# Optimization experiments

Measured on AMD Instinct MI355X. Metric: run time of the kernel, lower is better.

Reference implementation:

```python
import jax, jax.numpy as jnp
import numpy as np

B, N, D_IN, D_OUT = 8, 2048, 256, 128
ROW_ZERO = 85 - 10  # hardcoded in original: a[:, 0:85-10] = 0 (zeros rows, dim 1)
NEG_BIG = -9.0e15
EPS = 1e-12  # F.normalize eps


def setup_inputs() -> dict:
    key = jax.random.key(0)
    k1, k2, k3, k4 = jax.random.split(key, 4)
    h = jax.random.normal(k1, (B, N, D_IN), dtype=jnp.float32)
    adj = jax.random.randint(k2, (B, N, N), 0, 2, dtype=jnp.int32)
    adj_eye = jax.random.randint(k3, (B, N, N), 0, 2, dtype=jnp.int32)
    # xavier_uniform with gain=1.414 for W [in, out]
    limit = 1.414 * np.sqrt(6.0 / (D_IN + D_OUT))
    W = jax.random.uniform(k4, (D_IN, D_OUT), minval=-limit, maxval=limit, dtype=jnp.float32)
    return {"h": h, "adj": adj, "adj_eye": adj_eye, "W": W}


def reference(h, adj, adj_eye, W):
    # Wh: [B, N, D_OUT]
    Wh = jnp.matmul(h, W)
    # L2-normalize along feature dim (F.normalize semantics: x / max(||x||, eps))
    norm = jnp.maximum(jnp.linalg.norm(Wh, axis=-1, keepdims=True), EPS)
    Whn = Wh / norm
    # dense cosine-similarity scores: [B, N, N]
    score = jnp.einsum("bnd,bmd->bnm", Whn, Whn)
    # double-sort top-k emulation (faithful to original, incl. row-wise zeroing bug)
    a_sorted = jnp.sort(score, axis=-1)
    idx1 = jnp.argsort(score, axis=-1)
    a_sorted = a_sorted.at[:, 0:ROW_ZERO, :].set(0.0)
    idx2 = jnp.argsort(idx1, axis=-1)  # inverse permutation
    attscore = jnp.take_along_axis(a_sorted, idx2, axis=-1)
    # adjacency mask + softmax over neighbors
    e = jnp.where(adj_eye > 0, attscore, NEG_BIG)
    attention = jax.nn.softmax(e, axis=-1)
    # (dropout is identity in eval mode)
    h_prime = jnp.matmul(attention, Wh)
    return jax.nn.elu(h_prime)
```

## Files before the change

kernel.cpp:

```cpp
#include <hip/hip_runtime.h>
#include <stdint.h>

#define NN   2048
#define DD   128
#define DIN  256
#define ROWZ 75

typedef float f32x4 __attribute__((ext_vector_type(4)));
typedef short bf16x8 __attribute__((ext_vector_type(8)));
typedef unsigned int u32x4 __attribute__((ext_vector_type(4)));
typedef unsigned int u32x2 __attribute__((ext_vector_type(2)));

__device__ __forceinline__ unsigned short f2bf(float x){
  union { float f; unsigned int u; } v; v.f = x;
  unsigned int u = v.u;
  u += 0x7fffu + ((u >> 16) & 1u);
  return (unsigned short)(u >> 16);
}
__device__ __forceinline__ float bf2f(unsigned short b){
  union { float f; unsigned int u; } v; v.u = ((unsigned int)b) << 16;
  return v.f;
}

__launch_bounds__(256, 2)
__global__ void wh_kernel(const float* __restrict__ h, const float* __restrict__ W,
                          unsigned short* __restrict__ whn, unsigned short* __restrict__ whT)
{
  __shared__ float hs[32][36];
  __shared__ float Ws[32][128];
  __shared__ float ssp[32][33];
  __shared__ float sinv[32];

  const int t  = threadIdx.x;
  const int r0 = blockIdx.x * 32;
  const int r4 = (t >> 5) * 4;
  const int d4 = (t & 31) * 4;

  float acc[4][4];
#pragma unroll
  for (int i = 0; i < 4; ++i)
#pragma unroll
    for (int j = 0; j < 4; ++j) acc[i][j] = 0.f;

  const int lrow = t >> 3;
  const int lkb  = (t & 7) * 4;

  for (int kt = 0; kt < 8; ++kt){
    __syncthreads();
    {
      const float* src = h + (size_t)(r0 + lrow) * DIN + kt * 32 + lkb;
      f32x4 a = *(const f32x4*)src;
#pragma unroll
      for (int e = 0; e < 4; ++e) hs[lkb + e][lrow] = a[e];
    }
    {
      const int k = t >> 3;
      const int d = (t & 7) * 16;
      const float* src = W + (size_t)(kt * 32 + k) * DD + d;
      float* dst = &Ws[k][d];
#pragma unroll
      for (int e = 0; e < 4; ++e) ((f32x4*)dst)[e] = ((const f32x4*)src)[e];
    }
    __syncthreads();
#pragma unroll
    for (int k = 0; k < 32; ++k){
      f32x4 w4 = *(const f32x4*)&Ws[k][d4];
      f32x4 ha = *(const f32x4*)&hs[k][r4];
#pragma unroll
      for (int i = 0; i < 4; ++i)
#pragma unroll
        for (int j = 0; j < 4; ++j)
          acc[i][j] += ha[i] * w4[j];
    }
  }

#pragma unroll
  for (int i = 0; i < 4; ++i){
    float s = acc[i][0]*acc[i][0] + acc[i][1]*acc[i][1]
            + acc[i][2]*acc[i][2] + acc[i][3]*acc[i][3];
    ssp[r4 + i][t & 31] = s;
  }
  __syncthreads();
  if (t < 32){
    float ss = 0.f;
#pragma unroll
    for (int c = 0; c < 32; ++c) ss += ssp[t][c];
    sinv[t] = 1.0f / fmaxf(sqrtf(ss), 1e-12f);
  }
  __syncthreads();

  const int bb = r0 >> 11;
  const int n0 = (r0 & 2047) + r4;

#pragma unroll
  for (int i = 0; i < 4; ++i){
    const float inv = sinv[r4 + i];
    unsigned int lo = (unsigned int)f2bf(acc[i][0]*inv) | ((unsigned int)f2bf(acc[i][1]*inv) << 16);
    unsigned int hi = (unsigned int)f2bf(acc[i][2]*inv) | ((unsigned int)f2bf(acc[i][3]*inv) << 16);
    u32x2 pk = { lo, hi };
    *(u32x2*)(whn + (size_t)(r0 + r4 + i) * DD + d4) = pk;
  }
#pragma unroll
  for (int j = 0; j < 4; ++j){
    u32x2 pk;
#pragma unroll
    for (int e = 0; e < 2; ++e)
      pk[e] = (unsigned int)f2bf(acc[2*e][j]) | ((unsigned int)f2bf(acc[2*e + 1][j]) << 16);
    *(u32x2*)(whT + ((size_t)(bb * DD + d4 + j)) * NN + n0) = pk;
  }
}

__launch_bounds__(256, 2)
__global__ void attn_kernel(const unsigned short* __restrict__ whn,
                            const unsigned short* __restrict__ whT,
                            const int* __restrict__ adj,
                            float* __restrict__ out)
{
  __shared__ unsigned short Vt[128 * 128];
  __shared__ unsigned short Pbuf[4][32 * 40];
  __shared__ float linv_s[32];

  const int t    = threadIdx.x;
  const int w    = t >> 6;
  const int l    = t & 63;
  const int quad = l >> 4;
  const int l16  = l & 15;
  const int b    = blockIdx.x >> 6;
  const int qbase = (blockIdx.x & 63) * 32;

  const unsigned short* whn_b = whn + (size_t)b * NN * DD;
  const unsigned short* whT_b = whT + (size_t)b * DD * NN;
  const int*            adj_b = adj + (size_t)b * NN * NN;

  bf16x8 qf[2][4];
#pragma unroll
  for (int s = 0; s < 2; ++s)
#pragma unroll
    for (int kc = 0; kc < 4; ++kc)
      qf[s][kc] = *(const bf16x8*)(whn_b + (size_t)(qbase + s*16 + l16) * DD + kc*32 + quad*8);

  f32x4 oacc[2][8];
  float lacc[2][4];
#pragma unroll
  for (int s = 0; s < 2; ++s){
#pragma unroll
    for (int dt = 0; dt < 8; ++dt) oacc[s][dt] = (f32x4){0.f, 0.f, 0.f, 0.f};
#pragma unroll
    for (int r = 0; r < 4; ++r) lacc[s][r] = 0.f;
  }

  unsigned short* const Pw = &Pbuf[w][0];

  int av[2][2][4];
#pragma unroll
  for (int f = 0; f < 2; ++f)
#pragma unroll
    for (int s = 0; s < 2; ++s)
#pragma unroll
      for (int r = 0; r < 4; ++r)
        av[f][s][r] = adj_b[(size_t)(qbase + s*16 + quad*4 + r) * NN + w*32 + f*16 + l16];

  for (int it = 0; it < 16; ++it){
    const int m0 = it * 128;
    __syncthreads();

#pragma unroll
    for (int ii = 0; ii < 8; ++ii){
      const int d   = w*32 + ii*4 + quad;
      const int gsw = l16 ^ (d & 7);
      const unsigned short* src = whT_b + (size_t)d * NN + m0 + gsw * 8;
      __builtin_amdgcn_global_load_lds(
          (const __attribute__((address_space(1))) void*)src,
          (__attribute__((address_space(3))) void*)&Vt[(w*32 + ii*4) * 128],
          16, 0, 0);
    }

    int av_n[2][2][4];
    {
      const int mnext = (it < 15) ? (m0 + 128) : 0;
#pragma unroll
      for (int f = 0; f < 2; ++f)
#pragma unroll
        for (int s = 0; s < 2; ++s)
#pragma unroll
          for (int r = 0; r < 4; ++r)
            av_n[f][s][r] = adj_b[(size_t)(qbase + s*16 + quad*4 + r) * NN + mnext + w*32 + f*16 + l16];
    }

    bf16x8 kf[2][4];
#pragma unroll
    for (int f = 0; f < 2; ++f)
#pragma unroll
      for (int kc = 0; kc < 4; ++kc)
        kf[f][kc] = *(const bf16x8*)(whn_b + (size_t)(m0 + w*32 + f*16 + l16) * DD + kc*32 + quad*8);

#pragma unroll
    for (int f = 0; f < 2; ++f){
#pragma unroll
      for (int s = 0; s < 2; ++s){
        f32x4 sc = (f32x4){0.f, 0.f, 0.f, 0.f};
#pragma unroll
        for (int kc = 0; kc < 4; ++kc)
          sc = __builtin_amdgcn_mfma_f32_16x16x32_bf16(qf[s][kc], kf[f][kc], sc, 0, 0, 0);
#pragma unroll
        for (int r = 0; r < 4; ++r){
          const int qrow = qbase + s*16 + quad*4 + r;
          float sv = (qrow < ROWZ) ? 0.f : sc[r];
          float p32 = (av[f][s][r] > 0) ? __expf(sv) : 0.f;
          unsigned short pb = f2bf(p32);
          lacc[s][r] += bf2f(pb);
          Pw[(s*16 + quad*4 + r) * 40 + f*16 + l16] = pb;
        }
      }
    }
    __syncthreads();

#pragma unroll
    for (int s = 0; s < 2; ++s){
      bf16x8 pfr = *(const bf16x8*)&Pw[(s*16 + l16) * 40 + quad*8];
#pragma unroll
      for (int dt = 0; dt < 8; ++dt){
        const int d  = dt*16 + l16;
        const int gg = (w*4 + quad) ^ (d & 7);
        bf16x8 vf = *(const bf16x8*)&Vt[d * 128 + gg * 8];
        oacc[s][dt] = __builtin_amdgcn_mfma_f32_16x16x32_bf16(pfr, vf, oacc[s][dt], 0, 0, 0);
      }
    }

#pragma unroll
    for (int f = 0; f < 2; ++f)
#pragma unroll
      for (int s = 0; s < 2; ++s)
#pragma unroll
        for (int r = 0; r < 4; ++r)
          av[f][s][r] = av_n[f][s][r];
  }

  {
    float* lredw = (float*)Pw;
#pragma unroll
    for (int s = 0; s < 2; ++s)
#pragma unroll
      for (int r = 0; r < 4; ++r)
        lredw[(s*16 + quad*4 + r) * 16 + l16] = lacc[s][r];
  }
  __syncthreads();
  if (t < 32){
    float sum = 0.f;
    for (int ww = 0; ww < 4; ++ww){
      const float* lr = (const float*)&Pbuf[ww][0];
#pragma unroll
      for (int c = 0; c < 16; ++c) sum += lr[t * 16 + c];
    }
    linv_s[t] = 1.0f / sum;
  }

  float* const ored = (float*)&Vt[0];
  for (int s = 0; s < 2; ++s){
    __syncthreads();
#pragma unroll
    for (int dt = 0; dt < 8; ++dt)
#pragma unroll
      for (int r = 0; r < 4; ++r)
        ored[w*2048 + (quad*4 + r)*128 + dt*16 + l16] = oacc[s][dt][r];
    __syncthreads();
#pragma unroll
    for (int j = 0; j < 8; ++j){
      const int o  = j*256 + t;
      const int ql = o >> 7, d = o & 127;
      float v = ored[ql*128 + d] + ored[2048 + ql*128 + d]
              + ored[4096 + ql*128 + d] + ored[6144 + ql*128 + d];
      v *= linv_s[s*16 + ql];
      v = (v > 0.f) ? v : expm1f(v);
      out[(size_t)(b*NN + qbase + s*16 + ql) * DD + d] = v;
    }
  }
}

extern "C" void kernel_launch(void* const* d_in, const int* in_sizes, int n_in,
                              void* d_out, int out_size, void* d_ws, size_t ws_size,
                              hipStream_t stream)
{
  const float* h       = (const float*)d_in[0];
  const int*   adj_eye = (const int*)d_in[2];
  const float* W       = (const float*)d_in[3];
  float*       out     = (float*)d_out;

  unsigned short* whn = (unsigned short*)d_ws;
  unsigned short* whT = whn + (size_t)16384 * 128;

  wh_kernel<<<512, 256, 0, stream>>>(h, W, whn, whT);
  attn_kernel<<<512, 256, 0, stream>>>(whn, whT, adj_eye, out);
}
```

Baseline: 298.5 us.

## Restructure attention kernel so each wave owns 16 query rows over all keys

The attention kernel now launches 128-thread blocks in which each wave processes 16 query rows independently across all 2048 keys, in 32-key steps. The V^T fragments now come straight from global memory into registers with software prefetch, replacing the shared-memory Vt staging, and adjacency values are prefetched two steps ahead. This removes block-wide barriers and the cross-wave partial-output reduction in shared memory, and interleaves batches across block indices. In exchange, each wave reloads K and V from global/L2 with no sharing between waves, which raises memory traffic and register pressure.

```diff
diff --git a/kernel.cpp b/kernel.cpp
--- a/kernel.cpp
+++ b/kernel.cpp
@@ -110,171 +110,136 @@
   }
 }
 
-__launch_bounds__(256, 2)
+__launch_bounds__(128, 2)
 __global__ void attn_kernel(const unsigned short* __restrict__ whn,
                             const unsigned short* __restrict__ whT,
                             const int* __restrict__ adj,
                             float* __restrict__ out)
 {
-  __shared__ unsigned short Vt[128 * 128];
-  __shared__ unsigned short Pbuf[4][32 * 40];
-  __shared__ float linv_s[32];
+  __shared__ unsigned short Pbuf[2][16 * 40];
 
   const int t    = threadIdx.x;
   const int w    = t >> 6;
   const int l    = t & 63;
   const int quad = l >> 4;
   const int l16  = l & 15;
-  const int b    = blockIdx.x >> 6;
-  const int qbase = (blockIdx.x & 63) * 32;
+  const int b    = blockIdx.x & 7;
+  const int qt   = blockIdx.x >> 3;
+  const int q0   = qt * 32 + w * 16;
 
   const unsigned short* whn_b = whn + (size_t)b * NN * DD;
   const unsigned short* whT_b = whT + (size_t)b * DD * NN;
   const int*            adj_b = adj + (size_t)b * NN * NN;
 
-  bf16x8 qf[2][4];
-#pragma unroll
-  for (int s = 0; s < 2; ++s)
+  bf16x8 qf[4];
+#pragma unroll
+  for (int kc = 0; kc < 4; ++kc)
+    qf[kc] = *(const bf16x8*)(whn_b + (size_t)(q0 + l16) * DD + kc*32 + quad*8);
+
+  f32x4 oacc[8];
+  float lacc[4];
+#pragma unroll
+  for (int dt = 0; dt < 8; ++dt) oacc[dt] = (f32x4){0.f, 0.f, 0.f, 0.f};
+#pragma unroll
+  for (int r = 0; r < 4; ++r) lacc[r] = 0.f;
+
+  const int arow = q0 + quad*4;
+
+  int av0[2][4], av1[2][4];
+#pragma unroll
+  for (int f = 0; f < 2; ++f)
+#pragma unroll
+    for (int r = 0; r < 4; ++r){
+      av0[f][r] = adj_b[(size_t)(arow + r) * NN +  0 + f*16 + l16];
+      av1[f][r] = adj_b[(size_t)(arow + r) * NN + 32 + f*16 + l16];
+    }
+  bf16x8 kf0[2][4], vf0[8];
+#pragma unroll
+  for (int f = 0; f < 2; ++f)
 #pragma unroll
     for (int kc = 0; kc < 4; ++kc)
-      qf[s][kc] = *(const bf16x8*)(whn_b + (size_t)(qbase + s*16 + l16) * DD + kc*32 + quad*8);
-
-  f32x4 oacc[2][8];
-  float lacc[2][4];
-#pragma unroll
-  for (int s = 0; s < 2; ++s){
-#pragma unroll
-    for (int dt = 0; dt < 8; ++dt) oacc[s][dt] = (f32x4){0.f, 0.f, 0.f, 0.f};
-#pragma unroll
-    for (int r = 0; r < 4; ++r) lacc[s][r] = 0.f;
-  }
+      kf0[f][kc] = *(const bf16x8*)(whn_b + (size_t)(f*16 + l16) * DD + kc*32 + quad*8);
+#pragma unroll
+  for (int dt = 0; dt < 8; ++dt)
+    vf0[dt] = *(const bf16x8*)(whT_b + (size_t)(dt*16 + l16) * NN + quad*8);
 
   unsigned short* const Pw = &Pbuf[w][0];
 
-  int av[2][2][4];
-#pragma unroll
-  for (int f = 0; f < 2; ++f)
-#pragma unroll
-    for (int s = 0; s < 2; ++s)
+  for (int it = 0; it < 64; ++it){
+    const int m0 = it * 32;
+    const int mn = (m0 + 32) & 2047;
+    const int ma = (m0 + 64) & 2047;
+
+    bf16x8 kfn[2][4], vfn[8];
+    int avn[2][4];
+#pragma unroll
+    for (int f = 0; f < 2; ++f)
+#pragma unroll
+      for (int kc = 0; kc < 4; ++kc)
+        kfn[f][kc] = *(const bf16x8*)(whn_b + (size_t)(mn + f*16 + l16) * DD + kc*32 + quad*8);
+#pragma unroll
+    for (int dt = 0; dt < 8; ++dt)
+      vfn[dt] = *(const bf16x8*)(whT_b + (size_t)(dt*16 + l16) * NN + mn + quad*8);
+#pragma unroll
+    for (int f = 0; f < 2; ++f)
 #pragma unroll
       for (int r = 0; r < 4; ++r)
-        av[f][s][r] = adj_b[(size_t)(qbase + s*16 + quad*4 + r) * NN + w*32 + f*16 + l16];
-
-  for (int it = 0; it < 16; ++it){
-    const int m0 = it * 128;
-    __syncthreads();
-
-#pragma unroll
-    for (int ii = 0; ii < 8; ++ii){
-      const int d   = w*32 + ii*4 + quad;
-      const int gsw = l16 ^ (d & 7);
-      const unsigned short* src = whT_b + (size_t)d * NN + m0 + gsw * 8;
-      __builtin_amdgcn_global_load_lds(
-          (const __attribute__((address_space(1))) void*)src,
-          (__attribute__((address_space(3))) void*)&Vt[(w*32 + ii*4) * 128],
-          16, 0, 0);
-    }
-
-    int av_n[2][2][4];
+        avn[f][r] = adj_b[(size_t)(arow + r) * NN + ma + f*16 + l16];
+
+#pragma unroll
+    for (int f = 0; f < 2; ++f){
+      f32x4 sc = (f32x4){0.f, 0.f, 0.f, 0.f};
+#pragma unroll
+      for (int kc = 0; kc < 4; ++kc)
+        sc = __builtin_amdgcn_mfma_f32_16x16x32_bf16(qf[kc], kf0[f][kc], sc, 0, 0, 0);
+#pragma unroll
+      for (int r = 0; r < 4; ++r){
+        const int qrow = arow + r;
+        float sv = (qrow < ROWZ) ? 0.f : sc[r];
+        float p32 = (av0[f][r] > 0) ? __expf(sv) : 0.f;
+        unsigned short pb = f2bf(p32);
+        lacc[r] += bf2f(pb);
+        Pw[(quad*4 + r) * 40 + f*16 + l16] = pb;
+      }
+    }
+
     {
-      const int mnext = (it < 15) ? (m0 + 128) : 0;
-#pragma unroll
-      for (int f = 0; f < 2; ++f)
-#pragma unroll
-        for (int s = 0; s < 2; ++s)
-#pragma unroll
-          for (int r = 0; r < 4; ++r)
-            av_n[f][s][r] = adj_b[(size_t)(qbase + s*16 + quad*4 + r) * NN + mnext + w*32 + f*16 + l16];
-    }
-
-    bf16x8 kf[2][4];
-#pragma unroll
-    for (int f = 0; f < 2; ++f)
-#pragma unroll
-      for (int kc = 0; kc < 4; ++kc)
-        kf[f][kc] = *(const bf16x8*)(whn_b + (size_t)(m0 + w*32 + f*16 + l16) * DD + kc*32 + quad*8);
+      bf16x8 pf = *(const bf16x8*)&Pw[l16 * 40 + quad*8];
+#pragma unroll
+      for (int dt = 0; dt < 8; ++dt)
+        oacc[dt] = __builtin_amdgcn_mfma_f32_16x16x32_bf16(pf, vf0[dt], oacc[dt], 0, 0, 0);
+    }
 
 #pragma unroll
     for (int f = 0; f < 2; ++f){
 #pragma unroll
-      for (int s = 0; s < 2; ++s){
-        f32x4 sc = (f32x4){0.f, 0.f, 0.f, 0.f};
-#pragma unroll
-        for (int kc = 0; kc < 4; ++kc)
-          sc = __builtin_amdgcn_mfma_f32_16x16x32_bf16(qf[s][kc], kf[f][kc], sc, 0, 0, 0);
-#pragma unroll
-        for (int r = 0; r < 4; ++r){
-          const int qrow = qbase + s*16 + quad*4 + r;
-          float sv = (qrow < ROWZ) ? 0.f : sc[r];
-          float p32 = (av[f][s][r] > 0) ? __expf(sv) : 0.f;
-          unsigned short pb = f2bf(p32);
-          lacc[s][r] += bf2f(pb);
-          Pw[(s*16 + quad*4 + r) * 40 + f*16 + l16] = pb;
-        }
-      }
-    }
-    __syncthreads();
-
-#pragma unroll
-    for (int s = 0; s < 2; ++s){
-      bf16x8 pfr = *(const bf16x8*)&Pw[(s*16 + l16) * 40 + quad*8];
-#pragma unroll
-      for (int dt = 0; dt < 8; ++dt){
-        const int d  = dt*16 + l16;
-        const int gg = (w*4 + quad) ^ (d & 7);
-        bf16x8 vf = *(const bf16x8*)&Vt[d * 128 + gg * 8];
-        oacc[s][dt] = __builtin_amdgcn_mfma_f32_16x16x32_bf16(pfr, vf, oacc[s][dt], 0, 0, 0);
-      }
-    }
-
-#pragma unroll
-    for (int f = 0; f < 2; ++f)
-#pragma unroll
-      for (int s = 0; s < 2; ++s)
-#pragma unroll
-        for (int r = 0; r < 4; ++r)
-          av[f][s][r] = av_n[f][s][r];
-  }
-
-  {
-    float* lredw = (float*)Pw;
-#pragma unroll
-    for (int s = 0; s < 2; ++s)
-#pragma unroll
-      for (int r = 0; r < 4; ++r)
-        lredw[(s*16 + quad*4 + r) * 16 + l16] = lacc[s][r];
-  }
-  __syncthreads();
-  if (t < 32){
-    float sum = 0.f;
-    for (int ww = 0; ww < 4; ++ww){
-      const float* lr = (const float*)&Pbuf[ww][0];
-#pragma unroll
-      for (int c = 0; c < 16; ++c) sum += lr[t * 16 + c];
-    }
-    linv_s[t] = 1.0f / sum;
-  }
-
-  float* const ored = (float*)&Vt[0];
-  for (int s = 0; s < 2; ++s){
-    __syncthreads();
-#pragma unroll
-    for (int dt = 0; dt < 8; ++dt)
-#pragma unroll
-      for (int r = 0; r < 4; ++r)
-        ored[w*2048 + (quad*4 + r)*128 + dt*16 + l16] = oacc[s][dt][r];
-    __syncthreads();
-#pragma unroll
-    for (int j = 0; j < 8; ++j){
-      const int o  = j*256 + t;
-      const int ql = o >> 7, d = o & 127;
-      float v = ored[ql*128 + d] + ored[2048 + ql*128 + d]
-              + ored[4096 + ql*128 + d] + ored[6144 + ql*128 + d];
-      v *= linv_s[s*16 + ql];
+      for (int kc = 0; kc < 4; ++kc) kf0[f][kc] = kfn[f][kc];
+#pragma unroll
+      for (int r = 0; r < 4; ++r){ av0[f][r] = av1[f][r]; av1[f][r] = avn[f][r]; }
+    }
+#pragma unroll
+    for (int dt = 0; dt < 8; ++dt) vf0[dt] = vfn[dt];
+  }
+
+  float linv[4];
+#pragma unroll
+  for (int r = 0; r < 4; ++r){
+    float s = lacc[r];
+    s += __shfl_xor(s, 1);
+    s += __shfl_xor(s, 2);
+    s += __shfl_xor(s, 4);
+    s += __shfl_xor(s, 8);
+    linv[r] = 1.0f / s;
+  }
+
+#pragma unroll
+  for (int dt = 0; dt < 8; ++dt)
+#pragma unroll
+    for (int r = 0; r < 4; ++r){
+      float v = oacc[dt][r] * linv[r];
       v = (v > 0.f) ? v : expm1f(v);
-      out[(size_t)(b*NN + qbase + s*16 + ql) * DD + d] = v;
-    }
-  }
+      out[((size_t)b * NN + q0 + quad*4 + r) * DD + dt*16 + l16] = v;
+    }
 }
 
 extern "C" void kernel_launch(void* const* d_in, const int* in_sizes, int n_in,
@@ -290,5 +255,5 @@
   unsigned short* whT = whn + (size_t)16384 * 128;
 
   wh_kernel<<<512, 256, 0, stream>>>(h, W, whn, whT);
-  attn_kernel<<<512, 256, 0, stream>>>(whn, whT, adj_eye, out);
-}
+  attn_kernel<<<512, 128, 0, stream>>>(whn, whT, adj_eye, out);
+}
```

New measurement: 372.2 us. 24.7% more time.

## Preload adjacency rows as ballot bitmasks into shared memory before main loop

Applied to the files above, without the earlier changes.

Each block now reads its 32 adjacency rows up front with fully coalesced 64-wide loads, packs them into per-row bitmasks via wavefront ballots, and stores them in LDS. The main loop then tests a bit per score instead of issuing scattered per-lane int loads prefetched one iteration ahead. This replaces strided 16-lane global loads with contiguous ones and frees registers, but it front-loads all adjacency traffic before compute with no overlap, and adds about 8.7KB of LDS per block.

```diff
diff --git a/kernel.cpp b/kernel.cpp
--- a/kernel.cpp
+++ b/kernel.cpp
@@ -118,6 +118,7 @@
 {
   __shared__ unsigned short Vt[128 * 128];
   __shared__ unsigned short Pbuf[4][32 * 40];
+  __shared__ unsigned int   Ms[32 * 68];
   __shared__ float linv_s[32];
 
   const int t    = threadIdx.x;
@@ -132,6 +133,24 @@
   const unsigned short* whT_b = whT + (size_t)b * DD * NN;
   const int*            adj_b = adj + (size_t)b * NN * NN;
 
+  {
+    const int rbase = qbase + w * 8;
+    for (int c = 0; c < 32; ++c){
+      int a[8];
+#pragma unroll
+      for (int j = 0; j < 8; ++j)
+        a[j] = adj_b[(size_t)(rbase + j) * NN + c*64 + l];
+#pragma unroll
+      for (int j = 0; j < 8; ++j){
+        unsigned long long bb = __ballot(a[j] > 0);
+        if (l < 2){
+          unsigned int val = (l & 1) ? (unsigned int)(bb >> 32) : (unsigned int)bb;
+          Ms[(w*8 + j) * 68 + c*2 + l] = val;
+        }
+      }
+    }
+  }
+
   bf16x8 qf[2][4];
 #pragma unroll
   for (int s = 0; s < 2; ++s)
@@ -150,15 +169,6 @@
   }
 
   unsigned short* const Pw = &Pbuf[w][0];
-
-  int av[2][2][4];
-#pragma unroll
-  for (int f = 0; f < 2; ++f)
-#pragma unroll
-    for (int s = 0; s < 2; ++s)
-#pragma unroll
-      for (int r = 0; r < 4; ++r)
-        av[f][s][r] = adj_b[(size_t)(qbase + s*16 + quad*4 + r) * NN + w*32 + f*16 + l16];
 
   for (int it = 0; it < 16; ++it){
     const int m0 = it * 128;
@@ -175,18 +185,6 @@
           16, 0, 0);
     }
 
-    int av_n[2][2][4];
-    {
-      const int mnext = (it < 15) ? (m0 + 128) : 0;
-#pragma unroll
-      for (int f = 0; f < 2; ++f)
-#pragma unroll
-        for (int s = 0; s < 2; ++s)
-#pragma unroll
-          for (int r = 0; r < 4; ++r)
-            av_n[f][s][r] = adj_b[(size_t)(qbase + s*16 + quad*4 + r) * NN + mnext + w*32 + f*16 + l16];
-    }
-
     bf16x8 kf[2][4];
 #pragma unroll
     for (int f = 0; f < 2; ++f)
@@ -194,25 +192,34 @@
       for (int kc = 0; kc < 4; ++kc)
         kf[f][kc] = *(const bf16x8*)(whn_b + (size_t)(m0 + w*32 + f*16 + l16) * DD + kc*32 + quad*8);
 
-#pragma unroll
-    for (int f = 0; f < 2; ++f){
+    f32x4 sc[2][2];
+#pragma unroll
+    for (int f = 0; f < 2; ++f)
 #pragma unroll
       for (int s = 0; s < 2; ++s){
-        f32x4 sc = (f32x4){0.f, 0.f, 0.f, 0.f};
+        f32x4 a = (f32x4){0.f, 0.f, 0.f, 0.f};
 #pragma unroll
         for (int kc = 0; kc < 4; ++kc)
-          sc = __builtin_amdgcn_mfma_f32_16x16x32_bf16(qf[s][kc], kf[f][kc], sc, 0, 0, 0);
-#pragma unroll
-        for (int r = 0; r < 4; ++r){
-          const int qrow = qbase + s*16 + quad*4 + r;
-          float sv = (qrow < ROWZ) ? 0.f : sc[r];
-          float p32 = (av[f][s][r] > 0) ? __expf(sv) : 0.f;
+          a = __builtin_amdgcn_mfma_f32_16x16x32_bf16(qf[s][kc], kf[f][kc], a, 0, 0, 0);
+        sc[f][s] = a;
+      }
+
+    const int uidx = (m0 >> 5) + w;
+#pragma unroll
+    for (int s = 0; s < 2; ++s)
+#pragma unroll
+      for (int r = 0; r < 4; ++r){
+        const unsigned int mv = Ms[(s*16 + quad*4 + r) * 68 + uidx];
+        const int qrow = qbase + s*16 + quad*4 + r;
+#pragma unroll
+        for (int f = 0; f < 2; ++f){
+          float sv  = (qrow < ROWZ) ? 0.f : sc[f][s][r];
+          float p32 = ((mv >> (f*16 + l16)) & 1u) ? __expf(sv) : 0.f;
           unsigned short pb = f2bf(p32);
           lacc[s][r] += bf2f(pb);
           Pw[(s*16 + quad*4 + r) * 40 + f*16 + l16] = pb;
         }
       }
-    }
     __syncthreads();
 
 #pragma unroll
@@ -226,14 +233,6 @@
         oacc[s][dt] = __builtin_amdgcn_mfma_f32_16x16x32_bf16(pfr, vf, oacc[s][dt], 0, 0, 0);
       }
     }
-
-#pragma unroll
-    for (int f = 0; f < 2; ++f)
-#pragma unroll
-      for (int s = 0; s < 2; ++s)
-#pragma unroll
-        for (int r = 0; r < 4; ++r)
-          av[f][s][r] = av_n[f][s][r];
   }
 
   {
@@ -286,8 +285,8 @@
   const float* W       = (const float*)d_in[3];
   float*       out     = (float*)d_out;
 
-  unsigned short* whn = (unsigned short*)d_ws;
-  unsigned short* whT = whn + (size_t)16384 * 128;
+  unsigned short* whn  = (unsigned short*)d_ws;
+  unsigned short* whT  = whn + (size_t)16384 * 128;
 
   wh_kernel<<<512, 256, 0, stream>>>(h, W, whn, whT);
   attn_kernel<<<512, 256, 0, stream>>>(whn, whT, adj_eye, out);
```

After: 324.3 us. 8.6% more time.
